# Kernel optimization log

Measured on AMD Instinct MI355X. Metric: run time of the kernel, lower is better.

The kernel has to match this reference:

```python
import jax, jax.numpy as jnp
import numpy as np

E, N, D_IN, HID, TD, H = 800000, 50000, 64, 32, 32, 4
HO = H * HID
VOCAB = 1000000


def time_encode(t, dim):
    # t: [E,1] -> [E,dim], interleaved sin/cos harmonic encoding
    div_term = jnp.exp(jnp.arange(0, dim, 2, dtype=jnp.float32) * (-jnp.log(10000.0) / dim))
    ang = t * div_term  # [E, dim//2]
    return jnp.stack([jnp.sin(ang), jnp.cos(ang)], axis=-1).reshape(t.shape[0], dim)


def tgat_conv(x, src, dst, t_feat, wq, bq, wk, bk, wv, bv, wt, bt, num_nodes):
    # x: [N, Fin]; t_feat: [E, TD]
    q = (x @ wq + bq).reshape(-1, H, HID)
    k = (x @ wk + bk).reshape(-1, H, HID)
    v = (x @ wv + bv).reshape(-1, H, HID)
    te = (t_feat @ wt + bt).reshape(-1, H, HID)
    q_i = q[dst]                      # [E,H,HID] gather at target
    k_j = k[src] + te                 # [E,H,HID] gather at source + time enc
    alpha = jnp.sum(q_i * k_j, axis=-1) / jnp.sqrt(jnp.float32(HID))  # [E,H]
    # segment softmax over edges grouped by destination node
    m = jax.ops.segment_max(alpha, dst, num_segments=num_nodes)        # [N,H]
    ex = jnp.exp(alpha - m[dst])
    s = jax.ops.segment_sum(ex, dst, num_segments=num_nodes)           # [N,H]
    a = ex / (s[dst] + 1e-16)                                          # [E,H]
    msg = v[src] * a[:, :, None]                                       # [E,H,HID]
    out = jax.ops.segment_sum(msg, dst, num_segments=num_nodes)        # [N,H,HID]
    return out.reshape(num_nodes, HO)


def setup_inputs() -> dict:
    key = jax.random.key(0)
    ks = jax.random.split(key, 24)

    def lin_w(k, fi, fo):
        return jax.random.normal(k, (fi, fo), dtype=jnp.float32) / jnp.sqrt(jnp.float32(fi))

    inp = {
        'edge_index': jax.random.randint(ks[0], (2, E), 0, N),
        'edge_attr': jax.random.uniform(ks[1], (E, 2), dtype=jnp.float32),
        'num_nodes': N,
        'emb': jax.random.normal(ks[2], (VOCAB, D_IN), dtype=jnp.float32) * 0.1,
        'wq1': lin_w(ks[3], D_IN, HO), 'bq1': jnp.zeros((HO,), jnp.float32),
        'wk1': lin_w(ks[4], D_IN, HO), 'bk1': jnp.zeros((HO,), jnp.float32),
        'wv1': lin_w(ks[5], D_IN, HO), 'bv1': jnp.zeros((HO,), jnp.float32),
        'wt1': lin_w(ks[6], TD, HO), 'bt1': jnp.zeros((HO,), jnp.float32),
        'wq2': lin_w(ks[7], HO, HO), 'bq2': jnp.zeros((HO,), jnp.float32),
        'wk2': lin_w(ks[8], HO, HO), 'bk2': jnp.zeros((HO,), jnp.float32),
        'wv2': lin_w(ks[9], HO, HO), 'bv2': jnp.zeros((HO,), jnp.float32),
        'wt2': lin_w(ks[10], TD, HO), 'bt2': jnp.zeros((HO,), jnp.float32),
        'wc': lin_w(ks[11], HO, 1), 'bc': jnp.zeros((1,), jnp.float32),
    }
    return inp


def reference(edge_index, edge_attr, num_nodes, emb,
              wq1, bq1, wk1, bk1, wv1, bv1, wt1, bt1,
              wq2, bq2, wk2, bk2, wv2, bv2, wt2, bt2,
              wc, bc):
    src, dst = edge_index[0], edge_index[1]
    x = emb[:num_nodes]                                   # node_emb(arange(N))
    raw_time = edge_attr[:, 1:2]                          # [E,1]
    t_feat = time_encode(raw_time, TD)                    # [E,TD]
    x = jax.nn.relu(tgat_conv(x, src, dst, t_feat, wq1, bq1, wk1, bk1, wv1, bv1, wt1, bt1, num_nodes))
    x = jax.nn.relu(tgat_conv(x, src, dst, t_feat, wq2, bq2, wk2, bk2, wv2, bv2, wt2, bt2, num_nodes))
    edge_emb = x[src] + x[dst]                            # [E,HO]
    return (edge_emb @ wc + bc).squeeze(-1)               # [E]
```

## Files before the change

kernel.cpp:

```cpp
#include <hip/hip_runtime.h>
#include <hip/hip_bf16.h>

#define NNODES 50000
#define HOUT   128
#define NHEAD  4
#define HID    32
#define TDIM   32

typedef _Float16 h8 __attribute__((ext_vector_type(8)));

__constant__ float DIVT[16] = {
    1.0f, 0.5623413251903491f, 0.31622776601683794f, 0.1778279410038923f,
    0.1f, 0.05623413251903491f, 0.03162277660168379f, 0.01778279410038923f,
    0.01f, 0.005623413251903491f, 0.003162277660168379f, 0.001778279410038923f,
    0.001f, 0.0005623413251903491f, 0.0003162277660168379f, 0.0001778279410038923f
};

__global__ __launch_bounds__(128) void prep_wqt_kernel(
    const float* __restrict__ wq, const float* __restrict__ bq,
    const float* __restrict__ wt, float* __restrict__ wqt,
    float* __restrict__ bqt, int din)
{
    __shared__ float wts[TDIM * HOUT];
    const int tid = threadIdx.x;
    for (int i = tid; i < TDIM * HOUT; i += 128) wts[i] = wt[i];
    __syncthreads();
    const int h = tid >> 5;
    const int t = tid & 31;
    const int d = blockIdx.x;
    const float* row = (d == din) ? bq : wq + (size_t)d * HOUT;
    float s = 0.f;
    #pragma unroll
    for (int d2 = 0; d2 < 32; d2++)
        s += row[h * 32 + d2] * wts[t * HOUT + h * 32 + d2];
    if (d == din) bqt[h * 32 + t] = s;
    else          wqt[(size_t)d * HOUT + h * 32 + t] = s;
}

__global__ __launch_bounds__(256) void gemm_qkv_kernel(
    const float* __restrict__ X, int din, int n,
    const float* __restrict__ W0, const float* __restrict__ W1,
    const float* __restrict__ W2, const float* __restrict__ W3,
    const float* __restrict__ B0, const float* __restrict__ B1,
    const float* __restrict__ B2, const float* __restrict__ B3,
    float* __restrict__ q, _Float16* __restrict__ kv, float* __restrict__ qwt)
{
    const int y = blockIdx.y;
    const float* W = (y == 0) ? W0 : (y == 1) ? W1 : (y == 2) ? W2 : W3;
    const float* B = (y == 0) ? B0 : (y == 1) ? B1 : (y == 2) ? B2 : B3;

    __shared__ float Xs[64 * 68];
    __shared__ float Ws[64 * HOUT];

    const int tid  = threadIdx.x;
    const int row0 = blockIdx.x * 64;
    const int rg   = tid >> 4;
    const int cg   = tid & 15;

    float acc[4][8];
    #pragma unroll
    for (int r = 0; r < 4; r++)
        #pragma unroll
        for (int c = 0; c < 8; c++) acc[r][c] = 0.f;

    const int ktiles = din >> 6;
    for (int kt = 0; kt < ktiles; kt++) {
        {
            const int lrow = tid >> 2;
            const int k0   = (tid & 3) << 4;
            const int grow = row0 + lrow;
            const float* src = X + (size_t)grow * din + kt * 64 + k0;
            #pragma unroll
            for (int i = 0; i < 4; i++) {
                float4 val = (grow < n) ? ((const float4*)src)[i]
                                        : make_float4(0.f, 0.f, 0.f, 0.f);
                *(float4*)&Xs[lrow * 68 + k0 + i * 4] = val;
            }
        }
        {
            const int k  = tid >> 2;
            const int c0 = (tid & 3) << 5;
            const float* src = W + (size_t)(kt * 64 + k) * HOUT + c0;
            #pragma unroll
            for (int i = 0; i < 8; i++)
                *(float4*)&Ws[k * HOUT + c0 + i * 4] = ((const float4*)src)[i];
        }
        __syncthreads();

        #pragma unroll 8
        for (int k = 0; k < 64; k++) {
            float4 b0 = *(const float4*)&Ws[k * HOUT + cg * 8];
            float4 b1 = *(const float4*)&Ws[k * HOUT + cg * 8 + 4];
            #pragma unroll
            for (int r = 0; r < 4; r++) {
                float a = Xs[(rg * 4 + r) * 68 + k];
                acc[r][0] += a * b0.x; acc[r][1] += a * b0.y;
                acc[r][2] += a * b0.z; acc[r][3] += a * b0.w;
                acc[r][4] += a * b1.x; acc[r][5] += a * b1.y;
                acc[r][6] += a * b1.z; acc[r][7] += a * b1.w;
            }
        }
        __syncthreads();
    }

    float4 bb0 = *(const float4*)&B[cg * 8];
    float4 bb1 = *(const float4*)&B[cg * 8 + 4];
    #pragma unroll
    for (int r = 0; r < 4; r++) {
        const int grow = row0 + rg * 4 + r;
        if (grow >= n) continue;
        float o[8] = {acc[r][0] + bb0.x, acc[r][1] + bb0.y, acc[r][2] + bb0.z,
                      acc[r][3] + bb0.w, acc[r][4] + bb1.x, acc[r][5] + bb1.y,
                      acc[r][6] + bb1.z, acc[r][7] + bb1.w};
        if (y == 0 || y == 3) {
            float* O = (y == 0) ? q : qwt;
            *(float4*)&O[(size_t)grow * HOUT + cg * 8]     = make_float4(o[0], o[1], o[2], o[3]);
            *(float4*)&O[(size_t)grow * HOUT + cg * 8 + 4] = make_float4(o[4], o[5], o[6], o[7]);
        } else {
            _Float16* O = kv + ((y == 1) ? 0 : 128);
            h8 hv;
            #pragma unroll
            for (int j = 0; j < 8; j++) hv[j] = (_Float16)o[j];
            *(h8*)&O[(size_t)grow * 256 + cg * 8] = hv;
        }
    }
}

__global__ __launch_bounds__(256) void hist_kernel(
    const int* __restrict__ ei, int* __restrict__ cnt, int E)
{
    const int e = blockIdx.x * 256 + threadIdx.x;
    if (e >= E) return;
    atomicAdd(&cnt[ei[E + e]], 1);
}

__global__ __launch_bounds__(1024) void scan_kernel(
    const int* __restrict__ cnt, int* __restrict__ off, int n)
{
    __shared__ int wsum[16];
    const int tid   = threadIdx.x;
    const int chunk = (n + 1023) >> 10;
    const int lo    = min(tid * chunk, n);
    const int hi    = min(lo + chunk, n);
    int s = 0;
    for (int i = lo; i < hi; i++) s += cnt[i];

    const int lane = tid & 63, wv = tid >> 6;
    int v = s;
    #pragma unroll
    for (int d = 1; d < 64; d <<= 1) {
        int t = __shfl_up(v, d);
        if (lane >= d) v += t;
    }
    if (lane == 63) wsum[wv] = v;
    __syncthreads();
    if (wv == 0 && lane < 16) {
        int w = wsum[lane];
        #pragma unroll
        for (int d = 1; d < 16; d <<= 1) {
            int t = __shfl_up(w, d);
            if (lane >= d) w += t;
        }
        wsum[lane] = w;
    }
    __syncthreads();
    int run = ((wv > 0) ? wsum[wv - 1] : 0) + (v - s);
    for (int i = lo; i < hi; i++) { off[i] = run; run += cnt[i]; }
    if (tid == 1023) off[n] = run;
}

__global__ __launch_bounds__(256) void scatter_kernel(
    const int* __restrict__ ei, const float* __restrict__ ea,
    const int* __restrict__ off, int* __restrict__ cur,
    int2* __restrict__ recs, int E)
{
    const int e = blockIdx.x * 256 + threadIdx.x;
    if (e >= E) return;
    const int dn = ei[E + e];
    const int pos = off[dn] + atomicAdd(&cur[dn], 1);
    recs[pos] = make_int2(ei[e], __float_as_int(ea[2 * e + 1]));
}

__global__ __launch_bounds__(256) void node_attn_kernel(
    const int* __restrict__ off, const int2* __restrict__ recs,
    const float* __restrict__ q, const _Float16* __restrict__ kv,
    const float* __restrict__ qwt, const float* __restrict__ bt,
    float* __restrict__ x, const float* __restrict__ wc,
    float* __restrict__ p, int n)
{
    const int wid = (blockIdx.x * 256 + threadIdx.x) >> 6;
    if (wid >= n) return;
    const int lane = threadIdx.x & 63;
    const int slot = lane >> 4;
    const int sub  = lane & 15;
    const int c0   = sub * 8;
    const int dn   = wid;

    const float4* qv = (const float4*)(q   + (size_t)dn * HOUT + c0);
    const float4* wv = (const float4*)(qwt + (size_t)dn * HOUT + c0);
    const float4 q0 = qv[0], q1 = qv[1];
    const float4 w0 = wv[0], w1 = wv[1];

    const float4 bt0 = ((const float4*)(bt + c0))[0];
    const float4 bt1 = ((const float4*)(bt + c0))[1];
    float qb = q0.x * bt0.x + q0.y * bt0.y + q0.z * bt0.z + q0.w * bt0.w +
               q1.x * bt1.x + q1.y * bt1.y + q1.z * bt1.z + q1.w * bt1.w;
    qb += __shfl_xor(qb, 1);
    qb += __shfl_xor(qb, 2);

    const int beg = off[dn];
    const int end = off[dn + 1];

    float acc[8] = {0.f, 0.f, 0.f, 0.f, 0.f, 0.f, 0.f, 0.f};
    float den = 0.f;

    for (int i = beg + slot; i < end; i += 4) {
        const int2 rec = recs[i];
        const int   sn = rec.x;
        const float rt = __int_as_float(rec.y);

        const h8 kk = *(const h8*)(kv + (size_t)sn * 256 + c0);
        const h8 vv = *(const h8*)(kv + (size_t)sn * 256 + 128 + c0);

        const int i0 = (sub & 3) * 4;
        float tf[8];
        #pragma unroll
        for (int jj = 0; jj < 4; jj++) {
            float s_, c_;
            __sincosf(rt * DIVT[i0 + jj], &s_, &c_);
            tf[2 * jj]     = s_;
            tf[2 * jj + 1] = c_;
        }

        float partial =
            q0.x * (float)kk[0] + q0.y * (float)kk[1] +
            q0.z * (float)kk[2] + q0.w * (float)kk[3] +
            q1.x * (float)kk[4] + q1.y * (float)kk[5] +
            q1.z * (float)kk[6] + q1.w * (float)kk[7] +
            w0.x * tf[0] + w0.y * tf[1] + w0.z * tf[2] + w0.w * tf[3] +
            w1.x * tf[4] + w1.y * tf[5] + w1.z * tf[6] + w1.w * tf[7];
        if ((sub & 3) == 0) partial += qb;

        partial += __shfl_xor(partial, 1);
        partial += __shfl_xor(partial, 2);

        const float ex = __expf(partial * 0.17677669529663687f);
        den += ex;
        #pragma unroll
        for (int j = 0; j < 8; j++) acc[j] += ex * (float)vv[j];
    }

    #pragma unroll
    for (int j = 0; j < 8; j++) {
        acc[j] += __shfl_xor(acc[j], 16);
        acc[j] += __shfl_xor(acc[j], 32);
    }
    den += __shfl_xor(den, 16);
    den += __shfl_xor(den, 32);

    if (lane < 16) {
        const float inv = 1.f / (den + 1e-16f);
        float o[8];
        #pragma unroll
        for (int j = 0; j < 8; j++) o[j] = fmaxf(acc[j] * inv, 0.f);
        if (p == nullptr) {
            float* xo = x + (size_t)dn * HOUT + c0;
            *(float4*)xo       = make_float4(o[0], o[1], o[2], o[3]);
            *((float4*)xo + 1) = make_float4(o[4], o[5], o[6], o[7]);
        } else {
            const float4 wc0 = ((const float4*)(wc + c0))[0];
            const float4 wc1 = ((const float4*)(wc + c0))[1];
            float pp = o[0] * wc0.x + o[1] * wc0.y + o[2] * wc0.z + o[3] * wc0.w +
                       o[4] * wc1.x + o[5] * wc1.y + o[6] * wc1.z + o[7] * wc1.w;
            pp += __shfl_xor(pp, 1);
            pp += __shfl_xor(pp, 2);
            pp += __shfl_xor(pp, 4);
            pp += __shfl_xor(pp, 8);
            if (sub == 0) p[dn] = pp;
        }
    }
}

__global__ __launch_bounds__(256) void edge_out_kernel(
    const int* __restrict__ ei, const float* __restrict__ p,
    const float* __restrict__ bc, float* __restrict__ out, int E)
{
    const int e = blockIdx.x * 256 + threadIdx.x;
    if (e >= E) return;
    out[e] = p[ei[e]] + p[ei[E + e]] + bc[0];
}

extern "C" void kernel_launch(void* const* d_in, const int* in_sizes, int n_in,
                              void* d_out, int out_size, void* d_ws, size_t ws_size,
                              hipStream_t stream)
{
    const int E = in_sizes[0] / 2;
    const int N = NNODES;

    const int*   ei  = (const int*)d_in[0];
    const float* ea  = (const float*)d_in[1];
    const float* emb = (const float*)d_in[3];
    const float *wq1 = (const float*)d_in[4],  *bq1 = (const float*)d_in[5];
    const float *wk1 = (const float*)d_in[6],  *bk1 = (const float*)d_in[7];
    const float *wv1 = (const float*)d_in[8],  *bv1 = (const float*)d_in[9];
    const float *wt1 = (const float*)d_in[10], *bt1 = (const float*)d_in[11];
    const float *wq2 = (const float*)d_in[12], *bq2 = (const float*)d_in[13];
    const float *wk2 = (const float*)d_in[14], *bk2 = (const float*)d_in[15];
    const float *wv2 = (const float*)d_in[16], *bv2 = (const float*)d_in[17];
    const float *wt2 = (const float*)d_in[18], *bt2 = (const float*)d_in[19];
    const float *wc  = (const float*)d_in[20], *bc  = (const float*)d_in[21];
    float* out = (float*)d_out;

    float* ws = (float*)d_ws;
    const size_t NF = (size_t)N * HOUT;
    float*     q    = ws;
    float*     qwt  = ws + NF;
    float*     xbuf = ws + 2 * NF;
    _Float16*  kv   = (_Float16*)(ws + 3 * NF);
    int2*      recs = (int2*)(ws + 4 * NF);
    float*     wqt1 = (float*)(recs + E);
    float*     wqt2 = wqt1 + 64 * HOUT;
    float*     bqt1 = wqt2 + 128 * HOUT;
    float*     bqt2 = bqt1 + HOUT;
    int*       cnt  = (int*)(bqt2 + HOUT);
    int*       off  = cnt + N;
    int*       cur  = off + N + 1;
    float*     p    = (float*)(cur + N);

    const dim3 ggemm((N + 63) / 64, 4);
    const int  eblk = (E + 255) / 256;
    const int  nblk = (N + 3) / 4;

    prep_wqt_kernel<<<65, 128, 0, stream>>>(wq1, bq1, wt1, wqt1, bqt1, 64);
    prep_wqt_kernel<<<129, 128, 0, stream>>>(wq2, bq2, wt2, wqt2, bqt2, 128);

    hipMemsetAsync(cnt, 0, (size_t)N * sizeof(int), stream);
    hipMemsetAsync(cur, 0, (size_t)N * sizeof(int), stream);
    hist_kernel<<<eblk, 256, 0, stream>>>(ei, cnt, E);
    scan_kernel<<<1, 1024, 0, stream>>>(cnt, off, N);
    scatter_kernel<<<eblk, 256, 0, stream>>>(ei, ea, off, cur, recs, E);

    gemm_qkv_kernel<<<ggemm, 256, 0, stream>>>(emb, 64, N,
        wq1, wk1, wv1, wqt1, bq1, bk1, bv1, bqt1, q, kv, qwt);
    node_attn_kernel<<<nblk, 256, 0, stream>>>(off, recs, q, kv, qwt, bt1,
                                               xbuf, nullptr, nullptr, N);

    gemm_qkv_kernel<<<ggemm, 256, 0, stream>>>(xbuf, 128, N,
        wq2, wk2, wv2, wqt2, bq2, bk2, bv2, bqt2, q, kv, qwt);
    node_attn_kernel<<<nblk, 256, 0, stream>>>(off, recs, q, kv, qwt, bt2,
                                               nullptr, wc, p, N);

    edge_out_kernel<<<(E + 255) / 256, 256, 0, stream>>>(ei, p, bc, out, E);
}
```

Measured before the change: 770.6 us.

## Precompute per-edge time encodings as fp16 in scatter and prefetch next edge

```diff
diff --git a/kernel.cpp b/kernel.cpp
--- a/kernel.cpp
+++ b/kernel.cpp
@@ -172,17 +172,32 @@
 __global__ __launch_bounds__(256) void scatter_kernel(
     const int* __restrict__ ei, const float* __restrict__ ea,
     const int* __restrict__ off, int* __restrict__ cur,
-    int2* __restrict__ recs, int E)
+    int* __restrict__ srcb, _Float16* __restrict__ tfb, int E)
 {
     const int e = blockIdx.x * 256 + threadIdx.x;
     if (e >= E) return;
     const int dn = ei[E + e];
+    const float rt = ea[2 * e + 1];
     const int pos = off[dn] + atomicAdd(&cur[dn], 1);
-    recs[pos] = make_int2(ei[e], __float_as_int(ea[2 * e + 1]));
+    srcb[pos] = ei[e];
+
+    _Float16 tfl[32];
+    #pragma unroll
+    for (int t = 0; t < 16; t++) {
+        float s_, c_;
+        __sincosf(rt * DIVT[t], &s_, &c_);
+        tfl[2 * t]     = (_Float16)s_;
+        tfl[2 * t + 1] = (_Float16)c_;
+    }
+    _Float16* dst = tfb + (size_t)pos * 32;
+    #pragma unroll
+    for (int j = 0; j < 4; j++)
+        *(h8*)(dst + j * 8) = *(h8*)(tfl + j * 8);
 }
 
 __global__ __launch_bounds__(256) void node_attn_kernel(
-    const int* __restrict__ off, const int2* __restrict__ recs,
+    const int* __restrict__ off, const int* __restrict__ srcb,
+    const _Float16* __restrict__ tfb,
     const float* __restrict__ q, const _Float16* __restrict__ kv,
     const float* __restrict__ qwt, const float* __restrict__ bt,
     float* __restrict__ x, const float* __restrict__ wc,
@@ -194,6 +209,7 @@
     const int slot = lane >> 4;
     const int sub  = lane & 15;
     const int c0   = sub * 8;
+    const int tf0  = (sub & 3) * 8;
     const int dn   = wid;
 
     const float4* qv = (const float4*)(q   + (size_t)dn * HOUT + c0);
@@ -214,22 +230,23 @@
     float acc[8] = {0.f, 0.f, 0.f, 0.f, 0.f, 0.f, 0.f, 0.f};
     float den = 0.f;
 
-    for (int i = beg + slot; i < end; i += 4) {
-        const int2 rec = recs[i];
-        const int   sn = rec.x;
-        const float rt = __int_as_float(rec.y);
-
+    int i = beg + slot;
+    int sn_n = 0; h8 tf_n = {};
+    if (i < end) {
+        sn_n = srcb[i];
+        tf_n = *(const h8*)(tfb + (size_t)i * 32 + tf0);
+    }
+
+    while (i < end) {
+        const int sn  = sn_n;
+        const h8 tfv  = tf_n;
         const h8 kk = *(const h8*)(kv + (size_t)sn * 256 + c0);
         const h8 vv = *(const h8*)(kv + (size_t)sn * 256 + 128 + c0);
 
-        const int i0 = (sub & 3) * 4;
-        float tf[8];
-        #pragma unroll
-        for (int jj = 0; jj < 4; jj++) {
-            float s_, c_;
-            __sincosf(rt * DIVT[i0 + jj], &s_, &c_);
-            tf[2 * jj]     = s_;
-            tf[2 * jj + 1] = c_;
+        const int j = i + 4;
+        if (j < end) {
+            sn_n = srcb[j];
+            tf_n = *(const h8*)(tfb + (size_t)j * 32 + tf0);
         }
 
         float partial =
@@ -237,8 +254,10 @@
             q0.z * (float)kk[2] + q0.w * (float)kk[3] +
             q1.x * (float)kk[4] + q1.y * (float)kk[5] +
             q1.z * (float)kk[6] + q1.w * (float)kk[7] +
-            w0.x * tf[0] + w0.y * tf[1] + w0.z * tf[2] + w0.w * tf[3] +
-            w1.x * tf[4] + w1.y * tf[5] + w1.z * tf[6] + w1.w * tf[7];
+            w0.x * (float)tfv[0] + w0.y * (float)tfv[1] +
+            w0.z * (float)tfv[2] + w0.w * (float)tfv[3] +
+            w1.x * (float)tfv[4] + w1.y * (float)tfv[5] +
+            w1.z * (float)tfv[6] + w1.w * (float)tfv[7];
         if ((sub & 3) == 0) partial += qb;
 
         partial += __shfl_xor(partial, 1);
@@ -247,7 +266,9 @@
         const float ex = __expf(partial * 0.17677669529663687f);
         den += ex;
         #pragma unroll
-        for (int j = 0; j < 8; j++) acc[j] += ex * (float)vv[j];
+        for (int jj = 0; jj < 8; jj++) acc[jj] += ex * (float)vv[jj];
+
+        i = j;
     }
 
     #pragma unroll
@@ -317,8 +338,9 @@
     float*     qwt  = ws + NF;
     float*     xbuf = ws + 2 * NF;
     _Float16*  kv   = (_Float16*)(ws + 3 * NF);
-    int2*      recs = (int2*)(ws + 4 * NF);
-    float*     wqt1 = (float*)(recs + E);
+    _Float16*  tfb  = (_Float16*)(ws + 4 * NF);
+    int*       srcb = (int*)(ws + 4 * NF + (size_t)16 * E);
+    float*     wqt1 = (float*)(srcb + E);
     float*     wqt2 = wqt1 + 64 * HOUT;
     float*     bqt1 = wqt2 + 128 * HOUT;
     float*     bqt2 = bqt1 + HOUT;
@@ -338,16 +360,16 @@
     hipMemsetAsync(cur, 0, (size_t)N * sizeof(int), stream);
     hist_kernel<<<eblk, 256, 0, stream>>>(ei, cnt, E);
     scan_kernel<<<1, 1024, 0, stream>>>(cnt, off, N);
-    scatter_kernel<<<eblk, 256, 0, stream>>>(ei, ea, off, cur, recs, E);
+    scatter_kernel<<<eblk, 256, 0, stream>>>(ei, ea, off, cur, srcb, tfb, E);
 
     gemm_qkv_kernel<<<ggemm, 256, 0, stream>>>(emb, 64, N,
         wq1, wk1, wv1, wqt1, bq1, bk1, bv1, bqt1, q, kv, qwt);
-    node_attn_kernel<<<nblk, 256, 0, stream>>>(off, recs, q, kv, qwt, bt1,
+    node_attn_kernel<<<nblk, 256, 0, stream>>>(off, srcb, tfb, q, kv, qwt, bt1,
                                                xbuf, nullptr, nullptr, N);
 
     gemm_qkv_kernel<<<ggemm, 256, 0, stream>>>(xbuf, 128, N,
         wq2, wk2, wv2, wqt2, bq2, bk2, bv2, bqt2, q, kv, qwt);
-    node_attn_kernel<<<nblk, 256, 0, stream>>>(off, recs, q, kv, qwt, bt2,
+    node_attn_kernel<<<nblk, 256, 0, stream>>>(off, srcb, tfb, q, kv, qwt, bt2,
                                                nullptr, wc, p, N);
 
     edge_out_kernel<<<(E + 255) / 256, 256, 0, stream>>>(ei, p, bc, out, E);
```

Result: slower. 787.6 us (+2.2%).
